# Optimization experiments

Hardware: AMD Instinct MI355X
Metric: run time of the kernel (lower is better)

Reference implementation:

```python
import jax, jax.numpy as jnp
import numpy as np

MICRO_BATCHES = 4
NUM_EXPERTS = 8  # world_size=1 -> num_local_experts = 8
EPS = 1e-5


def setup_inputs() -> dict:
    key = jax.random.key(0)
    ks = jax.random.split(key, 8)
    B, S, D = 8, 2048, 1024
    E, F = NUM_EXPERTS, 4 * D
    x = jax.random.normal(ks[0], (B, S, D), dtype=jnp.float32)
    gamma = jnp.ones((D,), jnp.float32)
    beta = jnp.zeros((D,), jnp.float32)
    gate_w = jax.random.normal(ks[1], (E, D), jnp.float32) * (1.0 / np.sqrt(D))
    w1 = jax.random.normal(ks[2], (E, D, F), jnp.float32) * (1.0 / np.sqrt(D))
    b1 = jnp.zeros((E, F), jnp.float32)
    w2 = jax.random.normal(ks[3], (E, F, D), jnp.float32) * (1.0 / np.sqrt(F))
    b2 = jnp.zeros((E, D), jnp.float32)
    return {"x": x, "gamma": gamma, "beta": beta, "gate_w": gate_w,
            "w1": w1, "b1": b1, "w2": w2, "b2": b2}


def reference(x, gamma, beta, gate_w, w1, b1, w2, b2):
    B, S, D = x.shape
    E = w1.shape[0]
    # micro-batch chunking along batch dim (chunk(MICRO_BATCHES, dim=0))
    xf = x.reshape(MICRO_BATCHES, -1, D)            # [MB, T, D], T = B/MB * S
    T = xf.shape[1]
    # residual (gated_input) is the pre-LN flat input
    # moe_norm: LayerNorm over last dim, biased variance, eps=1e-5
    mu = jnp.mean(xf, axis=-1, keepdims=True)
    var = jnp.mean(jnp.square(xf - mu), axis=-1, keepdims=True)
    xn = (xf - mu) * jax.lax.rsqrt(var + EPS) * gamma + beta  # [MB, T, D]
    # gate logits + topk are computed in the source but discarded
    _logits = jnp.einsum('mtd,ed->mte', xn, gate_w)
    _ = jax.lax.top_k(_logits, 2)
    # dispatch/combine are identity for world_size=1; tokens split round-robin
    # into num_local_experts contiguous chunks per micro-batch
    tpe = T // E
    xe = xn.reshape(MICRO_BATCHES, E, tpe, D)       # [MB, E, tpe, D]
    h = jax.nn.gelu(jnp.einsum('metd,edf->metf', xe, w1) + b1[None, :, None, :],
                    approximate=False)
    y = jnp.einsum('metf,efd->metd', h, w2) + b2[None, :, None, :]
    out = xf + y.reshape(MICRO_BATCHES, T, D)       # residual add
    return out.reshape(B, S, D)
```

## Files before the change

kernel.cpp:

```cpp
#include <hip/hip_runtime.h>
#include <stdint.h>
#include <math.h>

typedef unsigned short ushort_t;
typedef __attribute__((ext_vector_type(8))) short bf16x8;
typedef __attribute__((ext_vector_type(4))) float f32x4;

#define SLOT 32768
#define EPI_STRIDE 1032

__device__ __forceinline__ ushort_t f2bf(float f) {
  union { float f; unsigned u; } cv; cv.f = f;
  unsigned r = cv.u + 0x7fffu + ((cv.u >> 16) & 1u);
  return (ushort_t)(r >> 16);
}

__device__ __forceinline__ void gl_lds16(const void* g, void* l) {
  typedef __attribute__((address_space(1))) const char gchar;
  typedef __attribute__((address_space(3))) char lchar;
  __builtin_amdgcn_global_load_lds((gchar*)g, (lchar*)l, 16, 0, 0);
}

__device__ __forceinline__ f32x4 MFMA(bf16x8 a, bf16x8 b, f32x4 c) {
  return __builtin_amdgcn_mfma_f32_16x16x32_bf16(a, b, c, 0, 0, 0);
}

__global__ __launch_bounds__(256) void ln_kernel(const float* __restrict__ x,
                                                 const float* __restrict__ gamma,
                                                 const float* __restrict__ beta,
                                                 ushort_t* __restrict__ xn) {
  const int row = blockIdx.x;
  const int t = threadIdx.x;
  const float4 v = ((const float4*)(x + (size_t)row * 1024))[t];
  float s  = v.x + v.y + v.z + v.w;
  float ss = v.x * v.x + v.y * v.y + v.z * v.z + v.w * v.w;
#pragma unroll
  for (int o = 32; o >= 1; o >>= 1) {
    s  += __shfl_xor(s, o);
    ss += __shfl_xor(ss, o);
  }
  __shared__ float red[10];
  const int wave = t >> 6, lane = t & 63;
  if (lane == 0) { red[wave] = s; red[4 + wave] = ss; }
  __syncthreads();
  if (t == 0) {
    float S  = red[0] + red[1] + red[2] + red[3];
    float SS = red[4] + red[5] + red[6] + red[7];
    float mu  = S * (1.0f / 1024.0f);
    float var = SS * (1.0f / 1024.0f) - mu * mu;
    red[8] = mu;
    red[9] = rsqrtf(var + 1e-5f);
  }
  __syncthreads();
  const float mu = red[8], rs = red[9];
  const float4 g = ((const float4*)gamma)[t];
  const float4 b = ((const float4*)beta)[t];
  ushort4 o;
  o.x = f2bf((v.x - mu) * rs * g.x + b.x);
  o.y = f2bf((v.y - mu) * rs * g.y + b.y);
  o.z = f2bf((v.z - mu) * rs * g.z + b.z);
  o.w = f2bf((v.w - mu) * rs * g.w + b.w);
  ((ushort4*)(xn + (size_t)row * 1024))[t] = o;
}

__global__ __launch_bounds__(256) void transpose_cast(const float* __restrict__ in,
                                                      ushort_t* __restrict__ out,
                                                      int R, int C) {
  __shared__ float tile[32][33];
  const int e = blockIdx.z;
  const float* src = in + (size_t)e * R * C;
  ushort_t* dst = out + (size_t)e * R * C;
  const int c0 = blockIdx.x * 32, r0 = blockIdx.y * 32;
  const int tx = threadIdx.x, ty = threadIdx.y;
#pragma unroll
  for (int j = 0; j < 32; j += 8)
    tile[ty + j][tx] = src[(size_t)(r0 + ty + j) * C + c0 + tx];
  __syncthreads();
#pragma unroll
  for (int j = 0; j < 32; j += 8)
    dst[(size_t)(c0 + ty + j) * R + r0 + tx] = f2bf(tile[tx][ty + j]);
}


__device__ __forceinline__ void stage_half(const ushort_t* gsrc, int lda,
                                           char* half_base, int kt, int tid) {
  const int rr = tid >> 2;
  const int gs = (tid & 3) ^ ((tid >> 3) & 3);
  gl_lds16(gsrc + (size_t)rr * lda + kt + gs * 8, half_base + (tid >> 6) * 1024);
}

template <int BASE>
__device__ __forceinline__ void mfma16(const bf16x8 (&a)[4], const bf16x8 (&b)[4],
                                       f32x4 (&acc)[8][4]) {
  __builtin_amdgcn_s_setprio(1);
#pragma unroll
  for (int mi = 0; mi < 4; mi++)
#pragma unroll
    for (int ni = 0; ni < 4; ni++)
      acc[BASE + mi][ni] = MFMA(a[mi], b[ni], acc[BASE + mi][ni]);
  __builtin_amdgcn_s_setprio(0);
}

template <int VM, bool STG, bool LAST>
__device__ __forceinline__ void tile_body(char* smem, int T,
                                          const ushort_t* gA, const ushort_t* gB,
                                          int lda, int a_off, int b_off, int tid,
                                          bf16x8 (&bA0)[4], bf16x8 (&bA1)[4],
                                          bf16x8 (&bBc)[4], bf16x8 (&bBn)[4],
                                          f32x4 (&acc)[8][4]) {
  const char* slot = smem + (T & 3) * SLOT;
  char* nstg = smem + ((T + 3) & 3) * SLOT;
  const int kt3 = (T + 3) * 32;
#pragma unroll
  for (int mi = 0; mi < 4; mi++) bA1[mi] = *(const bf16x8*)(slot + a_off + (mi + 4) * 1024);
  if (STG) {
    stage_half(gA, lda, nstg, kt3, tid);
    stage_half(gA + (size_t)128 * lda, lda, nstg + 8192, kt3, tid);
  }
  __builtin_amdgcn_sched_barrier(0);
  __builtin_amdgcn_s_barrier();
  asm volatile("s_waitcnt lgkmcnt(0)" ::: "memory");
  __builtin_amdgcn_sched_barrier(0);
  mfma16<0>(bA0, bBc, acc);
  __builtin_amdgcn_sched_barrier(0);
  if (VM == 6)      asm volatile("s_waitcnt vmcnt(6)" ::: "memory");
  else if (VM == 4) asm volatile("s_waitcnt vmcnt(4)" ::: "memory");
  else if (VM == 0) asm volatile("s_waitcnt vmcnt(0)" ::: "memory");
  __builtin_amdgcn_s_barrier();
  if (!LAST) {
    const char* nslot = smem + ((T + 1) & 3) * SLOT;
#pragma unroll
    for (int ni = 0; ni < 4; ni++) bBn[ni] = *(const bf16x8*)(nslot + b_off + ni * 1024);
#pragma unroll
    for (int mi = 0; mi < 4; mi++) bA0[mi] = *(const bf16x8*)(nslot + a_off + mi * 1024);
  }
  if (STG) {
    stage_half(gB, lda, nstg + 16384, kt3, tid);
    stage_half(gB + (size_t)128 * lda, lda, nstg + 24576, kt3, tid);
  }
  __builtin_amdgcn_sched_barrier(0);
  __builtin_amdgcn_s_barrier();
  asm volatile("s_waitcnt lgkmcnt(0)" ::: "memory");
  __builtin_amdgcn_sched_barrier(0);
  mfma16<4>(bA1, bBc, acc);
  __builtin_amdgcn_sched_barrier(0);
  __builtin_amdgcn_s_barrier();
}

template <int EPI, int LDA, int LDC, int KTOT>
__global__ __launch_bounds__(512, 2) void gemm256(const ushort_t* __restrict__ A,
                                                  const ushort_t* __restrict__ Bw,
                                                  const float* __restrict__ bias,
                                                  const float* __restrict__ resid,
                                                  ushort_t* __restrict__ Hout,
                                                  float* __restrict__ Fout) {
  extern __shared__ char smem[];
  const int tid = threadIdx.x;
  const int wave = tid >> 6, lane = tid & 63;

  const int bid = blockIdx.x;
  const int c = bid & 7, l = bid >> 3;
  const int tm = c * 8 + (l & 7);
  const int tn = l >> 3;
  const int row0 = tm * 256;
  const int col0 = tn * 256;
  const int e = (row0 >> 9) & 7;

  const ushort_t* gA = A + (size_t)row0 * LDA;
  const ushort_t* gB = Bw + ((size_t)e * LDC + col0) * LDA;

  const int NT = KTOT / 32;

  const int wm = wave >> 2, wn = wave & 3;
  const int l15 = lane & 15, g = lane >> 4;
  const int sw = ((g ^ ((lane >> 1) & 3)) << 4);
  const int a_off = wm * 8192 + l15 * 64 + sw;
  const int b_off = 16384 + (wn >> 1) * 8192 + (wn & 1) * 4096 + l15 * 64 + sw;

  f32x4 acc[8][4] = {};
  bf16x8 bA0[4], bA1[4], bB0[4], bB1[4];

#pragma unroll
  for (int T = 0; T < 3; ++T) {
    char* s = smem + T * SLOT;
    stage_half(gA, LDA, s, T * 32, tid);
    stage_half(gA + (size_t)128 * LDA, LDA, s + 8192, T * 32, tid);
    stage_half(gB, LDA, s + 16384, T * 32, tid);
    stage_half(gB + (size_t)128 * LDA, LDA, s + 24576, T * 32, tid);
  }
  asm volatile("s_waitcnt vmcnt(8)" ::: "memory");
  __builtin_amdgcn_s_barrier();
#pragma unroll
  for (int ni = 0; ni < 4; ni++) bB0[ni] = *(const bf16x8*)(smem + b_off + ni * 1024);
#pragma unroll
  for (int mi = 0; mi < 4; mi++) bA0[mi] = *(const bf16x8*)(smem + a_off + mi * 1024);

  for (int T = 0; T < NT - 4; T += 2) {
    tile_body<6, true, false>(smem, T,     gA, gB, LDA, a_off, b_off, tid, bA0, bA1, bB0, bB1, acc);
    tile_body<6, true, false>(smem, T + 1, gA, gB, LDA, a_off, b_off, tid, bA0, bA1, bB1, bB0, acc);
  }
  tile_body<6, true,  false>(smem, NT - 4, gA, gB, LDA, a_off, b_off, tid, bA0, bA1, bB0, bB1, acc);
  tile_body<4, false, false>(smem, NT - 3, gA, gB, LDA, a_off, b_off, tid, bA0, bA1, bB1, bB0, acc);
  tile_body<0, false, false>(smem, NT - 2, gA, gB, LDA, a_off, b_off, tid, bA0, bA1, bB0, bB1, acc);
  tile_body<-1, false, true>(smem, NT - 1, gA, gB, LDA, a_off, b_off, tid, bA0, bA1, bB1, bB0, acc);

  __syncthreads();

  float bv[4];
#pragma unroll
  for (int ni = 0; ni < 4; ni++)
    bv[ni] = bias[e * LDC + col0 + wn * 64 + ni * 16 + l15];

#pragma unroll
  for (int r = 0; r < 4; ++r) {
#pragma unroll
    for (int mh = 0; mh < 2; ++mh) {
      const int mi = 2 * r + mh;
      const int lrow = wm * 32 + mh * 16 + g * 4;
#pragma unroll
      for (int ni = 0; ni < 4; ++ni) {
        const int colb = (wn * 64 + ni * 16 + l15) * 4;
#pragma unroll
        for (int rr = 0; rr < 4; ++rr) {
          float v = acc[mi][ni][rr] + bv[ni];
          if (EPI == 0) {
            float v2 = v * v;
            float cc = fmaf(0.044715f, v2, 1.0f);
            float u  = exp2f(-2.3022078f * v * cc);
            v = __fdividef(v, 1.0f + u);
          }
          *(float*)(smem + (size_t)(lrow + rr) * EPI_STRIDE + colb) = v;
        }
      }
    }
    __syncthreads();
#pragma unroll
    for (int i = 0; i < 8; ++i) {
      const int chunk = i * 512 + tid;
      const int lr = chunk >> 6;
      const int cb = (chunk & 63) * 16;
      const float4 v4 = *(const float4*)(smem + (size_t)lr * EPI_STRIDE + cb);
      const int grow = row0 + (lr < 32 ? r * 32 + lr : 128 + r * 32 + (lr - 32));
      const int gcol = col0 + (chunk & 63) * 4;
      if (EPI == 0) {
        ushort4 o;
        o.x = f2bf(v4.x); o.y = f2bf(v4.y); o.z = f2bf(v4.z); o.w = f2bf(v4.w);
        *(ushort4*)(&Hout[(size_t)grow * LDC + gcol]) = o;
      } else {
        const float4 rs = *(const float4*)(&resid[(size_t)grow * LDC + gcol]);
        float4 o;
        o.x = v4.x + rs.x; o.y = v4.y + rs.y; o.z = v4.z + rs.z; o.w = v4.w + rs.w;
        *(float4*)(&Fout[(size_t)grow * LDC + gcol]) = o;
      }
    }
    __syncthreads();
  }
}

extern "C" void kernel_launch(void* const* d_in, const int* in_sizes, int n_in,
                              void* d_out, int out_size, void* d_ws, size_t ws_size,
                              hipStream_t stream) {
  const float* x     = (const float*)d_in[0];
  const float* gamma = (const float*)d_in[1];
  const float* beta  = (const float*)d_in[2];
  const float* w1    = (const float*)d_in[4];
  const float* b1    = (const float*)d_in[5];
  const float* w2    = (const float*)d_in[6];
  const float* b2    = (const float*)d_in[7];
  float* out = (float*)d_out;

  char* ws = (char*)d_ws;
  ushort_t* xn  = (ushort_t*)ws;
  ushort_t* w1t = (ushort_t*)(ws + 33554432);
  ushort_t* w2t = (ushort_t*)(ws + 33554432 + 67108864);
  ushort_t* h   = (ushort_t*)(ws + 33554432 + 2 * 67108864);

  hipFuncSetAttribute(reinterpret_cast<const void*>(&gemm256<0, 1024, 4096, 1024>),
                      hipFuncAttributeMaxDynamicSharedMemorySize, 131072);
  hipFuncSetAttribute(reinterpret_cast<const void*>(&gemm256<1, 4096, 1024, 4096>),
                      hipFuncAttributeMaxDynamicSharedMemorySize, 131072);

  ln_kernel<<<16384, 256, 0, stream>>>(x, gamma, beta, xn);
  transpose_cast<<<dim3(128, 32, 8), dim3(32, 8), 0, stream>>>(w1, w1t, 1024, 4096);
  transpose_cast<<<dim3(32, 128, 8), dim3(32, 8), 0, stream>>>(w2, w2t, 4096, 1024);

  gemm256<0, 1024, 4096, 1024><<<dim3(1024), 512, 131072, stream>>>(xn, w1t, b1, nullptr, h, nullptr);
  gemm256<1, 4096, 1024, 4096><<<dim3(256), 512, 131072, stream>>>(h, w2t, b2, x, nullptr, out);
}
```

Measured before the change: 428.9 us.

## Restructure GEMM main loop with compile-time slot indices and fewer live fragment registers

```diff
diff --git a/kernel.cpp b/kernel.cpp
--- a/kernel.cpp
+++ b/kernel.cpp
@@ -101,18 +101,18 @@
   __builtin_amdgcn_s_setprio(0);
 }
 
-template <int VM, bool STG, bool LAST>
-__device__ __forceinline__ void tile_body(char* smem, int T,
+template <int SIDX, int VM, bool STG>
+__device__ __forceinline__ void slot_body(char* smem, int kt3,
                                           const ushort_t* gA, const ushort_t* gB,
                                           int lda, int a_off, int b_off, int tid,
-                                          bf16x8 (&bA0)[4], bf16x8 (&bA1)[4],
-                                          bf16x8 (&bBc)[4], bf16x8 (&bBn)[4],
                                           f32x4 (&acc)[8][4]) {
-  const char* slot = smem + (T & 3) * SLOT;
-  char* nstg = smem + ((T + 3) & 3) * SLOT;
-  const int kt3 = (T + 3) * 32;
-#pragma unroll
-  for (int mi = 0; mi < 4; mi++) bA1[mi] = *(const bf16x8*)(slot + a_off + (mi + 4) * 1024);
+  const char* slot = smem + SIDX * SLOT;
+  char* nstg = smem + ((SIDX + 3) & 3) * SLOT;
+  bf16x8 a[4], b[4];
+#pragma unroll
+  for (int ni = 0; ni < 4; ni++) b[ni] = *(const bf16x8*)(slot + b_off + ni * 1024);
+#pragma unroll
+  for (int mi = 0; mi < 4; mi++) a[mi] = *(const bf16x8*)(slot + a_off + mi * 1024);
   if (STG) {
     stage_half(gA, lda, nstg, kt3, tid);
     stage_half(gA + (size_t)128 * lda, lda, nstg + 8192, kt3, tid);
@@ -121,19 +121,11 @@
   __builtin_amdgcn_s_barrier();
   asm volatile("s_waitcnt lgkmcnt(0)" ::: "memory");
   __builtin_amdgcn_sched_barrier(0);
-  mfma16<0>(bA0, bBc, acc);
-  __builtin_amdgcn_sched_barrier(0);
-  if (VM == 6)      asm volatile("s_waitcnt vmcnt(6)" ::: "memory");
-  else if (VM == 4) asm volatile("s_waitcnt vmcnt(4)" ::: "memory");
-  else if (VM == 0) asm volatile("s_waitcnt vmcnt(0)" ::: "memory");
-  __builtin_amdgcn_s_barrier();
-  if (!LAST) {
-    const char* nslot = smem + ((T + 1) & 3) * SLOT;
-#pragma unroll
-    for (int ni = 0; ni < 4; ni++) bBn[ni] = *(const bf16x8*)(nslot + b_off + ni * 1024);
-#pragma unroll
-    for (int mi = 0; mi < 4; mi++) bA0[mi] = *(const bf16x8*)(nslot + a_off + mi * 1024);
-  }
+  mfma16<0>(a, b, acc);
+  __builtin_amdgcn_sched_barrier(0);
+  __builtin_amdgcn_s_barrier();
+#pragma unroll
+  for (int mi = 0; mi < 4; mi++) a[mi] = *(const bf16x8*)(slot + a_off + (mi + 4) * 1024);
   if (STG) {
     stage_half(gB, lda, nstg + 16384, kt3, tid);
     stage_half(gB + (size_t)128 * lda, lda, nstg + 24576, kt3, tid);
@@ -142,8 +134,11 @@
   __builtin_amdgcn_s_barrier();
   asm volatile("s_waitcnt lgkmcnt(0)" ::: "memory");
   __builtin_amdgcn_sched_barrier(0);
-  mfma16<4>(bA1, bBc, acc);
-  __builtin_amdgcn_sched_barrier(0);
+  mfma16<4>(a, b, acc);
+  __builtin_amdgcn_sched_barrier(0);
+  if (VM == 8)      asm volatile("s_waitcnt vmcnt(8)" ::: "memory");
+  else if (VM == 4) asm volatile("s_waitcnt vmcnt(4)" ::: "memory");
+  else if (VM == 0) asm volatile("s_waitcnt vmcnt(0)" ::: "memory");
   __builtin_amdgcn_s_barrier();
 }
 
@@ -178,7 +173,6 @@
   const int b_off = 16384 + (wn >> 1) * 8192 + (wn & 1) * 4096 + l15 * 64 + sw;
 
   f32x4 acc[8][4] = {};
-  bf16x8 bA0[4], bA1[4], bB0[4], bB1[4];
 
 #pragma unroll
   for (int T = 0; T < 3; ++T) {
@@ -190,19 +184,17 @@
   }
   asm volatile("s_waitcnt vmcnt(8)" ::: "memory");
   __builtin_amdgcn_s_barrier();
-#pragma unroll
-  for (int ni = 0; ni < 4; ni++) bB0[ni] = *(const bf16x8*)(smem + b_off + ni * 1024);
-#pragma unroll
-  for (int mi = 0; mi < 4; mi++) bA0[mi] = *(const bf16x8*)(smem + a_off + mi * 1024);
-
-  for (int T = 0; T < NT - 4; T += 2) {
-    tile_body<6, true, false>(smem, T,     gA, gB, LDA, a_off, b_off, tid, bA0, bA1, bB0, bB1, acc);
-    tile_body<6, true, false>(smem, T + 1, gA, gB, LDA, a_off, b_off, tid, bA0, bA1, bB1, bB0, acc);
-  }
-  tile_body<6, true,  false>(smem, NT - 4, gA, gB, LDA, a_off, b_off, tid, bA0, bA1, bB0, bB1, acc);
-  tile_body<4, false, false>(smem, NT - 3, gA, gB, LDA, a_off, b_off, tid, bA0, bA1, bB1, bB0, acc);
-  tile_body<0, false, false>(smem, NT - 2, gA, gB, LDA, a_off, b_off, tid, bA0, bA1, bB0, bB1, acc);
-  tile_body<-1, false, true>(smem, NT - 1, gA, gB, LDA, a_off, b_off, tid, bA0, bA1, bB1, bB0, acc);
+
+  for (int T = 0; T < NT - 4; T += 4) {
+    slot_body<0, 8, true>(smem, (T + 3) * 32, gA, gB, LDA, a_off, b_off, tid, acc);
+    slot_body<1, 8, true>(smem, (T + 4) * 32, gA, gB, LDA, a_off, b_off, tid, acc);
+    slot_body<2, 8, true>(smem, (T + 5) * 32, gA, gB, LDA, a_off, b_off, tid, acc);
+    slot_body<3, 8, true>(smem, (T + 6) * 32, gA, gB, LDA, a_off, b_off, tid, acc);
+  }
+  slot_body<0, 8, true >(smem, (NT - 1) * 32, gA, gB, LDA, a_off, b_off, tid, acc);
+  slot_body<1, 4, false>(smem, 0,             gA, gB, LDA, a_off, b_off, tid, acc);
+  slot_body<2, 0, false>(smem, 0,             gA, gB, LDA, a_off, b_off, tid, acc);
+  slot_body<3, -1, false>(smem, 0,            gA, gB, LDA, a_off, b_off, tid, acc);
 
   __syncthreads();
 
```

New measurement: 425.0 us. About the same (-0.9%).
